# Kernel tuning notes

Measured on AMD Instinct MI355X. Metric: run time of the kernel, lower is better.

## Reference

```python
import jax, jax.numpy as jnp
import numpy as np

N_NODES = 50000
N_EDGES = 800000
D_IN = 64
D_HID = 64
D_OUT = 64


def setup_inputs() -> dict:
    key = jax.random.key(0)
    ks = jax.random.split(key, 9)
    x = jax.random.normal(ks[0], (N_NODES, D_IN), dtype=jnp.float32)
    src = jax.random.randint(ks[1], (N_EDGES,), 0, N_NODES, dtype=jnp.int64)
    dst = jax.random.randint(ks[2], (N_EDGES,), 0, N_NODES, dtype=jnp.int64)
    s0 = 1.0 / np.sqrt(D_IN)
    s1 = 1.0 / np.sqrt(D_HID)
    W_self0 = jax.random.normal(ks[3], (D_IN, D_HID), dtype=jnp.float32) * s0
    W_neigh0 = jax.random.normal(ks[4], (D_IN, D_HID), dtype=jnp.float32) * s0
    b0 = jnp.zeros((D_HID,), dtype=jnp.float32)
    W_self1 = jax.random.normal(ks[5], (D_HID, D_OUT), dtype=jnp.float32) * s1
    W_neigh1 = jax.random.normal(ks[6], (D_HID, D_OUT), dtype=jnp.float32) * s1
    b1 = jnp.zeros((D_OUT,), dtype=jnp.float32)
    return {"x": x, "src": src, "dst": dst,
            "W_self0": W_self0, "W_neigh0": W_neigh0, "b0": b0,
            "W_self1": W_self1, "W_neigh1": W_neigh1, "b1": b1}


def reference(x, src, dst, W_self0, W_neigh0, b0, W_self1, W_neigh1, b1):
    n = x.shape[0]
    # in-degree per destination node; clamp to 1 for isolated nodes (DGL behavior)
    deg = jax.ops.segment_sum(jnp.ones(src.shape[0], dtype=x.dtype), dst, num_segments=n)
    inv_deg = (1.0 / jnp.maximum(deg, 1.0))[:, None]  # [N,1]

    def sage_mean(h, W_self, W_neigh, b):
        # gather src features, mean-reduce onto dst, then linear combine
        agg = jax.ops.segment_sum(h[src], dst, num_segments=n)  # [N,d]
        neigh = agg * inv_deg
        return h @ W_self + neigh @ W_neigh + b

    # layer 0: SAGEConv with internal relu activation
    h = jax.nn.relu(sage_mean(x, W_self0, W_neigh0, b0))
    # outer relu in GraphSAGE_Full.forward (idempotent after internal relu)
    h = jax.nn.relu(h)
    # dropout rate 0.0 -> identity
    # final layer: no activation
    h = sage_mean(h, W_self1, W_neigh1, b1)
    return h
```

## Files before the change

### kernel.cpp

```cpp
#include <hip/hip_runtime.h>

#define N_NODES 50000
#define N_EDGES 800000
#define D 64
#define NSLICE 4
#define SLICE_N ((N_NODES + NSLICE - 1) / NSLICE)
#define BCAP 64
#define XF_BLOCKS 512
#define PRE_XF_BLOCKS 768
#define PRE_FILL_BLOCKS 1280

__device__ __forceinline__ unsigned short f2bf(float f) {
    unsigned int u = __builtin_bit_cast(unsigned int, f);
    u += 0x7fffu + ((u >> 16) & 1u);
    return (unsigned short)(u >> 16);
}
__device__ __forceinline__ float bflo(unsigned int u) {
    return __builtin_bit_cast(float, u << 16);
}
__device__ __forceinline__ float bfhi(unsigned int u) {
    return __builtin_bit_cast(float, u & 0xffff0000u);
}

__device__ __forceinline__ void xform_body(const float* __restrict__ h,
        const float* __restrict__ Ws, const float* __restrict__ Wn,
        const float* __restrict__ b,
        float* __restrict__ yS, unsigned short* __restrict__ yN,
        int gwave, int nwaves, int lane) {
    int mat = gwave & 1;
    const float* W = mat ? Wn : Ws;

    float w[D];
#pragma unroll
    for (int k = 0; k < D; ++k) w[k] = W[k * D + lane];
    float bj = mat ? 0.f : b[lane];

    const int ngroups = (N_NODES + 3) / 4;
    for (int g = gwave >> 1; g < ngroups; g += (nwaves >> 1)) {
        const float* x0 = h + (size_t)(g * 4) * D;
        float a0 = bj, a1 = bj, a2 = bj, a3 = bj;
#pragma unroll
        for (int kq = 0; kq < 16; ++kq) {
            float4 v0 = *(const float4*)(x0 + 0 * D + kq * 4);
            float4 v1 = *(const float4*)(x0 + 1 * D + kq * 4);
            float4 v2 = *(const float4*)(x0 + 2 * D + kq * 4);
            float4 v3 = *(const float4*)(x0 + 3 * D + kq * 4);
            a0 = fmaf(v0.x, w[kq * 4 + 0], a0);
            a1 = fmaf(v1.x, w[kq * 4 + 0], a1);
            a2 = fmaf(v2.x, w[kq * 4 + 0], a2);
            a3 = fmaf(v3.x, w[kq * 4 + 0], a3);
            a0 = fmaf(v0.y, w[kq * 4 + 1], a0);
            a1 = fmaf(v1.y, w[kq * 4 + 1], a1);
            a2 = fmaf(v2.y, w[kq * 4 + 1], a2);
            a3 = fmaf(v3.y, w[kq * 4 + 1], a3);
            a0 = fmaf(v0.z, w[kq * 4 + 2], a0);
            a1 = fmaf(v1.z, w[kq * 4 + 2], a1);
            a2 = fmaf(v2.z, w[kq * 4 + 2], a2);
            a3 = fmaf(v3.z, w[kq * 4 + 2], a3);
            a0 = fmaf(v0.w, w[kq * 4 + 3], a0);
            a1 = fmaf(v1.w, w[kq * 4 + 3], a1);
            a2 = fmaf(v2.w, w[kq * 4 + 3], a2);
            a3 = fmaf(v3.w, w[kq * 4 + 3], a3);
        }
        size_t base = (size_t)(g * 4) * D + lane;
        if (mat) {
            yN[base + 0 * D] = f2bf(a0);
            yN[base + 1 * D] = f2bf(a1);
            yN[base + 2 * D] = f2bf(a2);
            yN[base + 3 * D] = f2bf(a3);
        } else {
            yS[base + 0 * D] = a0;
            yS[base + 1 * D] = a1;
            yS[base + 2 * D] = a2;
            yS[base + 3 * D] = a3;
        }
    }
}

__global__ __launch_bounds__(256) void k_pre(const float* __restrict__ x,
        const float* __restrict__ Ws0, const float* __restrict__ Wn0,
        const float* __restrict__ b0,
        float* __restrict__ yS, unsigned short* __restrict__ yN,
        const int* __restrict__ src, const int* __restrict__ dst,
        int* __restrict__ cnt, int* __restrict__ csr) {
    int bid = (int)blockIdx.x;
    if (bid < PRE_XF_BLOCKS) {
        int lane = threadIdx.x & 63;
        int gwave = __builtin_amdgcn_readfirstlane(bid * 4 + (int)(threadIdx.x >> 6));
        xform_body(x, Ws0, Wn0, b0, yS, yN, gwave, PRE_XF_BLOCKS * 4, lane);
    } else {
        int fid = bid - PRE_XF_BLOCKS;
        int slice = fid & 3;
        int lo = slice * SLICE_N, hi = lo + SLICE_N;
        int gblk = fid >> 2;
        const int4* d4p = (const int4*)dst;
        const int4* s4p = (const int4*)src;
        const int NV = N_EDGES / 4;
        const int STRIDE = (PRE_FILL_BLOCKS / 4) * 256;
        for (int v = gblk * 256 + (int)threadIdx.x; v < NV; v += STRIDE) {
            int4 d4 = d4p[v];
            int4 s4 = s4p[v];
            if (d4.x >= lo && d4.x < hi) { int p = atomicAdd(&cnt[d4.x], 1); csr[(d4.x << 6) + p] = s4.x; }
            if (d4.y >= lo && d4.y < hi) { int p = atomicAdd(&cnt[d4.y], 1); csr[(d4.y << 6) + p] = s4.y; }
            if (d4.z >= lo && d4.z < hi) { int p = atomicAdd(&cnt[d4.z], 1); csr[(d4.z << 6) + p] = s4.z; }
            if (d4.w >= lo && d4.w < hi) { int p = atomicAdd(&cnt[d4.w], 1); csr[(d4.w << 6) + p] = s4.w; }
        }
    }
}

__global__ __launch_bounds__(256) void k_xform(const float* __restrict__ h,
        const float* __restrict__ Ws, const float* __restrict__ Wn,
        const float* __restrict__ b,
        float* __restrict__ yS, unsigned short* __restrict__ yN) {
    int lane = threadIdx.x & 63;
    int gwave = __builtin_amdgcn_readfirstlane((int)((blockIdx.x * blockDim.x + threadIdx.x) >> 6));
    const int NW = (XF_BLOCKS * 256) >> 6;

    float ws[D], wn[D];
#pragma unroll
    for (int k = 0; k < D; ++k) ws[k] = Ws[k * D + lane];
#pragma unroll
    for (int k = 0; k < D; ++k) wn[k] = Wn[k * D + lane];
    float bj = b[lane];

    const int NG = N_NODES / 4;
    int g = gwave;
    if (g >= NG) return;
    uint4 xv = *(const uint4*)(h + (size_t)g * (4 * D) + lane * 4);
    for (; g < NG; g += NW) {
        int gn = g + NW; if (gn >= NG) gn = g;
        uint4 xn = *(const uint4*)(h + (size_t)gn * (4 * D) + lane * 4);
#pragma unroll
        for (int r = 0; r < 4; ++r) {
            float as = bj, an = 0.f;
#pragma unroll
            for (int k = 0; k < D; ++k) {
                unsigned comp = ((k & 3) == 0) ? xv.x : ((k & 3) == 1) ? xv.y
                              : ((k & 3) == 2) ? xv.z : xv.w;
                unsigned hb = (unsigned)__builtin_amdgcn_readlane((int)comp, (r << 4) | (k >> 2));
                float hk = __builtin_bit_cast(float, hb);
                as = fmaf(hk, ws[k], as);
                an = fmaf(hk, wn[k], an);
            }
            size_t row = (size_t)(g * 4 + r);
            yS[row * D + lane] = as;
            yN[row * D + lane] = f2bf(an);
        }
        xv = xn;
    }
}

__global__ __launch_bounds__(256) void k_aggf(const char* __restrict__ yN,
        const float* __restrict__ yS,
        const int* __restrict__ cnt, const int* __restrict__ csr,
        float* __restrict__ out, int relu) {
    int node = __builtin_amdgcn_readfirstlane((blockIdx.x * blockDim.x + threadIdx.x) >> 6);
    int lane = threadIdx.x & 63;
    int q = lane >> 3;
    int fq = lane & 7;
    int deg = cnt[node];
    const int* bucket = csr + (node << 6);
    unsigned foff = (unsigned)fq * 16u;

    float s0 = 0.f, s1 = 0.f, s2 = 0.f, s3 = 0.f;
    float s4 = 0.f, s5 = 0.f, s6 = 0.f, s7 = 0.f;

#define ROUND16(E0)                                                         \
    {                                                                       \
        int i0 = (E0) + q, i1 = i0 + 8;                                     \
        int b0 = bucket[i0], b1 = bucket[i1];                               \
        unsigned a0 = (i0 < deg) ? ((unsigned)b0 << 7) : 0u;                \
        unsigned a1 = (i1 < deg) ? ((unsigned)b1 << 7) : 0u;                \
        float m0 = (i0 < deg) ? 1.f : 0.f;                                  \
        float m1 = (i1 < deg) ? 1.f : 0.f;                                  \
        uint4 u0 = *(const uint4*)(yN + a0 + foff);                         \
        uint4 u1 = *(const uint4*)(yN + a1 + foff);                         \
        s0 = fmaf(m0, bflo(u0.x), s0); s0 = fmaf(m1, bflo(u1.x), s0);       \
        s1 = fmaf(m0, bfhi(u0.x), s1); s1 = fmaf(m1, bfhi(u1.x), s1);       \
        s2 = fmaf(m0, bflo(u0.y), s2); s2 = fmaf(m1, bflo(u1.y), s2);       \
        s3 = fmaf(m0, bfhi(u0.y), s3); s3 = fmaf(m1, bfhi(u1.y), s3);       \
        s4 = fmaf(m0, bflo(u0.z), s4); s4 = fmaf(m1, bflo(u1.z), s4);       \
        s5 = fmaf(m0, bfhi(u0.z), s5); s5 = fmaf(m1, bfhi(u1.z), s5);       \
        s6 = fmaf(m0, bflo(u0.w), s6); s6 = fmaf(m1, bflo(u1.w), s6);       \
        s7 = fmaf(m0, bfhi(u0.w), s7); s7 = fmaf(m1, bfhi(u1.w), s7);       \
    }

    ROUND16(0)
    ROUND16(16)
    if (deg > 32) {
        ROUND16(32)
        if (deg > 48) ROUND16(48)
    }
#undef ROUND16

    s0 += __shfl_xor(s0, 8, 64); s0 += __shfl_xor(s0, 16, 64); s0 += __shfl_xor(s0, 32, 64);
    s1 += __shfl_xor(s1, 8, 64); s1 += __shfl_xor(s1, 16, 64); s1 += __shfl_xor(s1, 32, 64);
    s2 += __shfl_xor(s2, 8, 64); s2 += __shfl_xor(s2, 16, 64); s2 += __shfl_xor(s2, 32, 64);
    s3 += __shfl_xor(s3, 8, 64); s3 += __shfl_xor(s3, 16, 64); s3 += __shfl_xor(s3, 32, 64);
    s4 += __shfl_xor(s4, 8, 64); s4 += __shfl_xor(s4, 16, 64); s4 += __shfl_xor(s4, 32, 64);
    s5 += __shfl_xor(s5, 8, 64); s5 += __shfl_xor(s5, 16, 64); s5 += __shfl_xor(s5, 32, 64);
    s6 += __shfl_xor(s6, 8, 64); s6 += __shfl_xor(s6, 16, 64); s6 += __shfl_xor(s6, 32, 64);
    s7 += __shfl_xor(s7, 8, 64); s7 += __shfl_xor(s7, 16, 64); s7 += __shfl_xor(s7, 32, 64);

    float sv = (q == 0) ? s0 : (q == 1) ? s1 : (q == 2) ? s2 : (q == 3) ? s3
             : (q == 4) ? s4 : (q == 5) ? s5 : (q == 6) ? s6 : s7;
    int f = fq * 8 + q;
    float self = yS[(size_t)node * D + f];
    float inv = 1.0f / fmaxf((float)deg, 1.0f);
    float acc = self + sv * inv;
    if (relu) acc = fmaxf(acc, 0.f);
    out[(size_t)node * D + f] = acc;
}

extern "C" void kernel_launch(void* const* d_in, const int* in_sizes, int n_in,
                              void* d_out, int out_size, void* d_ws, size_t ws_size,
                              hipStream_t stream) {
    const float* x   = (const float*)d_in[0];
    const int*   src = (const int*)d_in[1];
    const int*   dst = (const int*)d_in[2];
    const float* Ws0 = (const float*)d_in[3];
    const float* Wn0 = (const float*)d_in[4];
    const float* b0  = (const float*)d_in[5];
    const float* Ws1 = (const float*)d_in[6];
    const float* Wn1 = (const float*)d_in[7];
    const float* b1  = (const float*)d_in[8];
    float* out = (float*)d_out;

    char* p = (char*)d_ws;
    float*          yS  = (float*)p;          p += (size_t)N_NODES * D * sizeof(float);
    unsigned short* yN  = (unsigned short*)p; p += (size_t)N_NODES * D * sizeof(unsigned short);
    int* cnt = (int*)p;                       p += (size_t)N_NODES * sizeof(int);
    int* csr = (int*)p;                       p += (size_t)N_NODES * BCAP * sizeof(int);

    const int aggBlocks = (N_NODES + 3) / 4;

    hipMemsetAsync(cnt, 0, (size_t)N_NODES * sizeof(int), stream);

    k_pre<<<PRE_XF_BLOCKS + PRE_FILL_BLOCKS, 256, 0, stream>>>(
        x, Ws0, Wn0, b0, yS, yN, src, dst, cnt, csr);

    k_aggf<<<aggBlocks, 256, 0, stream>>>((const char*)yN, yS, cnt, csr, out, 1);

    k_xform<<<XF_BLOCKS, 256, 0, stream>>>(out, Ws1, Wn1, b1, yS, yN);
    k_aggf<<<aggBlocks, 256, 0, stream>>>((const char*)yN, yS, cnt, csr, out, 0);
}
```

Baseline: 183.6 us.

## Split transform waves by weight matrix to halve register use and triple grid

The node transform kernel now assigns each wavefront a single weight matrix (self or neighbor) instead of both, so it holds 64 weight registers rather than 128. The 4-row readlane broadcast and prefetch are replaced by one row per iteration, read through uniform scalar loads. The grid grows from 512 to 1536 blocks to raise occupancy. In exchange, each input row is loaded twice (once per matrix) and the explicit prefetch of the next row group is gone.

```diff
diff --git a/kernel.cpp b/kernel.cpp
--- a/kernel.cpp
+++ b/kernel.cpp
@@ -6,7 +6,7 @@
 #define NSLICE 4
 #define SLICE_N ((N_NODES + NSLICE - 1) / NSLICE)
 #define BCAP 64
-#define XF_BLOCKS 512
+#define XF_BLOCKS 1536
 #define PRE_XF_BLOCKS 768
 #define PRE_FILL_BLOCKS 1280
 
@@ -113,40 +113,23 @@
         const float* __restrict__ b,
         float* __restrict__ yS, unsigned short* __restrict__ yN) {
     int lane = threadIdx.x & 63;
-    int gwave = __builtin_amdgcn_readfirstlane((int)((blockIdx.x * blockDim.x + threadIdx.x) >> 6));
-    const int NW = (XF_BLOCKS * 256) >> 6;
-
-    float ws[D], wn[D];
-#pragma unroll
-    for (int k = 0; k < D; ++k) ws[k] = Ws[k * D + lane];
-#pragma unroll
-    for (int k = 0; k < D; ++k) wn[k] = Wn[k * D + lane];
-    float bj = b[lane];
-
-    const int NG = N_NODES / 4;
-    int g = gwave;
-    if (g >= NG) return;
-    uint4 xv = *(const uint4*)(h + (size_t)g * (4 * D) + lane * 4);
-    for (; g < NG; g += NW) {
-        int gn = g + NW; if (gn >= NG) gn = g;
-        uint4 xn = *(const uint4*)(h + (size_t)gn * (4 * D) + lane * 4);
-#pragma unroll
-        for (int r = 0; r < 4; ++r) {
-            float as = bj, an = 0.f;
-#pragma unroll
-            for (int k = 0; k < D; ++k) {
-                unsigned comp = ((k & 3) == 0) ? xv.x : ((k & 3) == 1) ? xv.y
-                              : ((k & 3) == 2) ? xv.z : xv.w;
-                unsigned hb = (unsigned)__builtin_amdgcn_readlane((int)comp, (r << 4) | (k >> 2));
-                float hk = __builtin_bit_cast(float, hb);
-                as = fmaf(hk, ws[k], as);
-                an = fmaf(hk, wn[k], an);
-            }
-            size_t row = (size_t)(g * 4 + r);
-            yS[row * D + lane] = as;
-            yN[row * D + lane] = f2bf(an);
-        }
-        xv = xn;
+    int wid = __builtin_amdgcn_readfirstlane((int)((blockIdx.x * blockDim.x + threadIdx.x) >> 6));
+    int mat = wid & 1;
+    const float* W = mat ? Wn : Ws;
+
+    float w[D];
+#pragma unroll
+    for (int k = 0; k < D; ++k) w[k] = W[k * D + lane];
+    float bj = mat ? 0.f : b[lane];
+
+    const int NWM = (XF_BLOCKS * 256 / 64) >> 1;
+    for (int row = wid >> 1; row < N_NODES; row += NWM) {
+        const float* hr = h + (size_t)row * D;
+        float acc = bj;
+#pragma unroll
+        for (int k = 0; k < D; ++k) acc = fmaf(hr[k], w[k], acc);
+        if (mat) yN[(size_t)row * D + lane] = f2bf(acc);
+        else     yS[(size_t)row * D + lane] = acc;
     }
 }
 
```

Measured after the change: 183.0 us. About the same (-0.3%).
